# Kernel tuning notes

Hardware: AMD Instinct MI355X
Metric: run time of the kernel (lower is better)

Reference implementation:

```python
import jax, jax.numpy as jnp
import numpy as np

# --- SLAYER hyperparameters (from netParams) ---
THETA = 10.0        # spike threshold
TAU_SR = 10.0       # SRM alpha-kernel time constant (ms)
TAU_RHO = 1.0       # surrogate-gradient width
SCALE_RHO = 1.0     # surrogate-gradient scale
TS = 1.0            # simulation step (ms)
T_SAMPLE = 300      # number of time steps
K_LEN = 64          # truncated SRM kernel length

N_BATCH, N_IN, N_HID, N_OUT = 128, 784, 410, 10


def srm_kernel():
    # SRM-alpha kernel eps(t) = (t/tau) * exp(1 - t/tau), sampled at Ts, eps(0)=0
    t = jnp.arange(K_LEN, dtype=jnp.float32) * TS
    return (t / TAU_SR) * jnp.exp(1.0 - t / TAU_SR)


def psp(x):
    # Causal FIR filtering along time: out[t] = sum_k eps[k] * x[t-k]
    # x: [N, C, T]
    n, c, t = x.shape
    kern = srm_kernel()
    lhs = x.reshape(n * c, 1, t)
    rhs = kern[::-1].reshape(1, 1, K_LEN)  # flip: conv_general_dilated is cross-correlation
    out = jax.lax.conv_general_dilated(
        lhs, rhs, window_strides=(1,), padding=[(K_LEN - 1, 0)],
        dimension_numbers=("NCH", "OIH", "NCH"))
    return out.reshape(n, c, t)


@jax.custom_vjp
def spike_fn(u):
    # Heaviside threshold with surrogate gradient rho(u) = (scale/tau) * exp(-|u-theta|/tau)
    return (u >= THETA).astype(u.dtype)

def _spike_fwd(u):
    return spike_fn(u), u

def _spike_bwd(u, g):
    return (g * (SCALE_RHO / TAU_RHO) * jnp.exp(-jnp.abs(u - THETA) / TAU_RHO),)

spike_fn.defvjp(_spike_fwd, _spike_bwd)


def setup_inputs() -> dict:
    key = jax.random.key(0)
    k1, k2, k3, k4 = jax.random.split(key, 4)
    img = jax.random.uniform(k1, (N_BATCH, N_IN), dtype=jnp.float32)
    rand_u = jax.random.uniform(k2, (N_BATCH, N_IN, T_SAMPLE), dtype=jnp.float32)
    W1 = jax.random.normal(k3, (N_HID, N_IN), dtype=jnp.float32)
    W2 = jax.random.normal(k4, (N_OUT, N_HID), dtype=jnp.float32)
    return {"img": img, "rand_u": rand_u, "W1": W1, "W2": W2}


def reference(img, rand_u, W1, W2):
    # Poisson spike encoding: spike whenever uniform noise < pixel intensity
    s0 = (rand_u < img[:, :, None]).astype(jnp.float32)        # [N, 784, T]
    # fc1 (dense over spatial features, shared over time) -> psp -> spike
    a1 = jnp.einsum("nit,oi->not", s0, W1)                     # [N, 410, T]
    s1 = spike_fn(psp(a1))
    # fc2 -> psp -> spike
    a2 = jnp.einsum("nht,oh->not", s1, W2)                     # [N, 10, T]
    s2 = spike_fn(psp(a2))
    return s2
```

## Files before the change

kernel.cpp:

```cpp
#include <hip/hip_runtime.h>
#include <cstdint>
#include <cstddef>

#define N_B 128
#define N_I 784
#define N_H 410
#define N_O 10
#define TT  300
#define KL  64
#define NW  26
#define NKS 13
#define NTILES 26
#define NDIG 4
#define NKS2 7
#define S1_TILE 4800
#define S1_NSTRIDE 134400
#define SEGL 19

typedef int v4i __attribute__((ext_vector_type(4)));

__device__ __forceinline__ uint32_t expand4(uint32_t v) {
  return (v * 0x00204081u) & 0x01010101u;
}

__global__ void k_pack(const float* __restrict__ rand_u, const float* __restrict__ img,
                       uint32_t* __restrict__ s0w) {
  int t = blockIdx.x * 64 + threadIdx.x;
  int w = blockIdx.y;
  int n = blockIdx.z;
  if (t >= TT) return;
  const float* rb = rand_u + (size_t)n * N_I * TT + t;
  const float* ib = img + (size_t)n * N_I;
  int ib32 = w * 32;
  float r[32];
  #pragma unroll
  for (int b = 0; b < 32; ++b) {
    int i = ib32 + b;
    r[b] = (i < N_I) ? rb[(size_t)i * TT] : 2.0f;
  }
  uint32_t bits = 0;
  #pragma unroll
  for (int b = 0; b < 32; ++b) {
    int i = ib32 + b;
    float p = (i < N_I) ? ib[i] : 0.0f;
    bits |= (r[b] < p ? 1u : 0u) << b;
  }
  s0w[((size_t)n * TT + t) * NW + w] = bits;
}

__global__ void k_bprepall(const float* __restrict__ W1, const float* __restrict__ W2,
                           v4i* __restrict__ Bf, v4i* __restrict__ Bf2) {
  int bid  = blockIdx.x;
  int lane = threadIdx.x;
  if (bid < NDIG * NTILES * NKS) {
    int ks   = bid % NKS;
    int rest = bid / NKS;
    int nt   = rest % NTILES;
    int d    = rest / NTILES;
    int o     = nt * 16 + (lane & 15);
    int kbase = ks * 64 + (lane >> 4) * 16;
    uint32_t wds[4] = {0, 0, 0, 0};
    for (int j = 0; j < 16; ++j) {
      int k = kbase + j;
      int dig = 0;
      if (o < N_H && k < N_I) {
        double w = (double)W1[(size_t)o * N_I + k];
        int r = (int)llround(w * 268435456.0);
        for (int dd = 0; dd <= d; ++dd) {
          dig = (int)(int8_t)(uint8_t)(r & 255);
          r = (r - dig) >> 8;
        }
      }
      wds[j >> 2] |= ((uint32_t)(uint8_t)(int8_t)dig) << (8 * (j & 3));
    }
    v4i v; v[0] = (int)wds[0]; v[1] = (int)wds[1]; v[2] = (int)wds[2]; v[3] = (int)wds[3];
    Bf[(size_t)bid * 64 + lane] = v;
  } else {
    int b2 = bid - NDIG * NTILES * NKS;
    int ks = b2 % NKS2, d = b2 / NKS2;
    int o     = lane & 15;
    int kbase = ks * 64 + (lane >> 4) * 16;
    uint32_t wds[4] = {0, 0, 0, 0};
    for (int j = 0; j < 16; ++j) {
      int k = kbase + j;
      int dig = 0;
      if (o < N_O && k < N_H) {
        double w = (double)W2[(size_t)o * N_H + k];
        int r = (int)llround(w * 268435456.0);
        for (int dd = 0; dd <= d; ++dd) {
          dig = (int)(int8_t)(uint8_t)(r & 255);
          r = (r - dig) >> 8;
        }
      }
      wds[j >> 2] |= ((uint32_t)(uint8_t)(int8_t)dig) << (8 * (j & 3));
    }
    v4i v; v[0] = (int)wds[0]; v[1] = (int)wds[1]; v[2] = (int)wds[2]; v[3] = (int)wds[3];
    Bf2[(size_t)b2 * 64 + lane] = v;
  }
}

__global__ __launch_bounds__(256) void k_fused2(const uint32_t* __restrict__ s0w,
                                                const v4i* __restrict__ Bf,
                                                uint8_t* __restrict__ s1) {
  __shared__ double tile[TT][17];
  int tid = threadIdx.x;
  int wave = tid >> 6, lane = tid & 63;
  int nt = blockIdx.x, n = blockIdx.y;
  int lrow = lane & 15, quad = lane >> 4;
  int wsel = quad >> 1, hsel = (quad & 1) * 16;
  const v4i* bb = Bf + (size_t)nt * NKS * 64 + lane;
  const size_t dstr = (size_t)NTILES * NKS * 64;
  const uint32_t* srow = s0w + (size_t)n * TT * NW;

  v4i acc[5][NDIG];
  #pragma unroll
  for (int mti = 0; mti < 5; ++mti)
    #pragma unroll
    for (int d = 0; d < NDIG; ++d) { acc[mti][d][0]=0; acc[mti][d][1]=0; acc[mti][d][2]=0; acc[mti][d][3]=0; }
  int rowc[5];
  #pragma unroll
  for (int mti = 0; mti < 5; ++mti) {
    int rr = wave * 80 + mti * 16 + lrow;
    rowc[mti] = (rr > TT - 1) ? TT - 1 : rr;
  }
  v4i bcur[NDIG]; uint32_t acur[5];
  #pragma unroll
  for (int d = 0; d < NDIG; ++d) bcur[d] = bb[(size_t)d * dstr];
  #pragma unroll
  for (int mti = 0; mti < 5; ++mti) acur[mti] = srow[(size_t)rowc[mti] * NW + wsel];
  for (int ks = 0; ks < NKS; ++ks) {
    int ks2 = (ks + 1 < NKS) ? ks + 1 : ks;
    v4i bnxt[NDIG]; uint32_t anxt[5];
    #pragma unroll
    for (int d = 0; d < NDIG; ++d) bnxt[d] = bb[(size_t)d * dstr + ks2 * 64];
    #pragma unroll
    for (int mti = 0; mti < 5; ++mti) anxt[mti] = srow[(size_t)rowc[mti] * NW + ks2 * 2 + wsel];
    #pragma unroll
    for (int mti = 0; mti < 5; ++mti) {
      uint32_t h = (acur[mti] >> hsel) & 0xFFFFu;
      v4i af;
      af[0] = (int)expand4(h & 0xF);
      af[1] = (int)expand4((h >> 4) & 0xF);
      af[2] = (int)expand4((h >> 8) & 0xF);
      af[3] = (int)expand4((h >> 12) & 0xF);
      #pragma unroll
      for (int d = 0; d < NDIG; ++d)
        acc[mti][d] = __builtin_amdgcn_mfma_i32_16x16x64_i8(af, bcur[d], acc[mti][d], 0, 0, 0);
    }
    #pragma unroll
    for (int d = 0; d < NDIG; ++d) bcur[d] = bnxt[d];
    #pragma unroll
    for (int mti = 0; mti < 5; ++mti) acur[mti] = anxt[mti];
  }
  #pragma unroll
  for (int mti = 0; mti < 5; ++mti)
    #pragma unroll
    for (int r = 0; r < 4; ++r) {
      int m = wave * 80 + mti * 16 + quad * 4 + r;
      if (m < TT) {
        double v = (double)acc[mti][0][r]
                 + 256.0      * (double)acc[mti][1][r]
                 + 65536.0    * (double)acc[mti][2][r]
                 + 16777216.0 * (double)acc[mti][3][r];
        tile[m][lrow] = v;
      }
    }
  __syncthreads();

  {
    int col = tid & 15;
    int seg = tid >> 4;
    int T0 = seg * SEGL;
    int Wc = T0 - 63; if (Wc < 0) Wc = 0;
    const double q   = exp(-0.1);
    const double q64 = exp(-6.4);
    const double cS  = (exp(1.0) / 10.0) * (1.0 / 268435456.0);
    double s1a = 0.0, s2a = 0.0, s1b = 0.0, s2b = 0.0;
    uint8_t* sb = s1 + (size_t)n * S1_NSTRIDE + (size_t)nt * S1_TILE + col;
    for (int j = 0; j < 63; ++j) {
      int t = T0 - 63 + j;
      int tc = (t < 0) ? 0 : t;
      double xa = (t >= 0) ? tile[tc][col] : 0.0;
      s2a = q * (s2a + s1a);
      s1a = q * s1a + xa;
    }
    for (int j = 0; j < SEGL; ++j) {
      int t = T0 + j;
      int tc = (t > TT - 1) ? TT - 1 : t;
      int tb = t - 64;
      int tbc = (tb < 0) ? 0 : tb;
      double xa = tile[tc][col];
      double xb = (tb >= Wc) ? tile[tbc][col] : 0.0;
      s2b = q * (s2b + s1b);
      s1b = q * s1b + xb;
      s2a = q * (s2a + s1a);
      s1a = q * s1a + xa;
      double y = cS * (s2a - q64 * (s2b + 64.0 * s1b));
      if (t < TT) sb[(size_t)t * 16] = (y >= 10.0) ? 1 : 0;
    }
  }
}

__global__ __launch_bounds__(256) void k_l2f(const uint8_t* __restrict__ s1,
                                             const v4i* __restrict__ Bf2,
                                             float* __restrict__ out) {
  __shared__ double tile2[TT][17];
  int tid = threadIdx.x;
  int wave = tid >> 6, lane = tid & 63;
  int n = blockIdx.x;
  int lrow = lane & 15, quad = lane >> 4;
  const uint8_t* s1n = s1 + (size_t)n * S1_NSTRIDE;
  for (int mt = wave; mt < 19; mt += 4) {
    int m0 = mt * 16;
    int trow = m0 + lrow; if (trow > TT - 1) trow = TT - 1;
    v4i acc[NDIG];
    #pragma unroll
    for (int d = 0; d < NDIG; ++d) { acc[d][0]=0; acc[d][1]=0; acc[d][2]=0; acc[d][3]=0; }
    for (int ks = 0; ks < NKS2; ++ks) {
      v4i af = *(const v4i*)(s1n + (size_t)(ks * 4 + quad) * S1_TILE + (size_t)trow * 16);
      #pragma unroll
      for (int d = 0; d < NDIG; ++d) {
        v4i bf = Bf2[(size_t)(d * NKS2 + ks) * 64 + lane];
        acc[d] = __builtin_amdgcn_mfma_i32_16x16x64_i8(af, bf, acc[d], 0, 0, 0);
      }
    }
    #pragma unroll
    for (int r = 0; r < 4; ++r) {
      int m = m0 + quad * 4 + r;
      if (m < TT && lrow < N_O) {
        double v = (double)acc[0][r]
                 + 256.0      * (double)acc[1][r]
                 + 65536.0    * (double)acc[2][r]
                 + 16777216.0 * (double)acc[3][r];
        tile2[m][lrow] = v;
      }
    }
  }
  __syncthreads();

  {
    int col = tid & 15;
    int seg = tid >> 4;
    int T0 = seg * SEGL;
    int Wc = T0 - 63; if (Wc < 0) Wc = 0;
    const double q   = exp(-0.1);
    const double q64 = exp(-6.4);
    const double cS  = (exp(1.0) / 10.0) * (1.0 / 268435456.0);
    double s1a = 0.0, s2a = 0.0, s1b = 0.0, s2b = 0.0;
    float* ob = out + (size_t)n * N_O * TT + (size_t)col * TT;
    for (int j = 0; j < 63; ++j) {
      int t = T0 - 63 + j;
      int tc = (t < 0) ? 0 : t;
      double xa = (t >= 0) ? tile2[tc][col] : 0.0;
      s2a = q * (s2a + s1a);
      s1a = q * s1a + xa;
    }
    for (int j = 0; j < SEGL; ++j) {
      int t = T0 + j;
      int tc = (t > TT - 1) ? TT - 1 : t;
      int tb = t - 64;
      int tbc = (tb < 0) ? 0 : tb;
      double xa = tile2[tc][col];
      double xb = (tb >= Wc) ? tile2[tbc][col] : 0.0;
      s2b = q * (s2b + s1b);
      s1b = q * s1b + xb;
      s2a = q * (s2a + s1a);
      s1a = q * s1a + xa;
      double y = cS * (s2a - q64 * (s2b + 64.0 * s1b));
      if (t < TT && col < N_O) ob[t] = (y >= 10.0) ? 1.0f : 0.0f;
    }
  }
}

extern "C" void kernel_launch(void* const* d_in, const int* in_sizes, int n_in,
                              void* d_out, int out_size, void* d_ws, size_t ws_size,
                              hipStream_t stream) {
  const float* img   = (const float*)d_in[0];
  const float* randu = (const float*)d_in[1];
  const float* W1    = (const float*)d_in[2];
  const float* W2    = (const float*)d_in[3];
  float* out = (float*)d_out;

  char* ws = (char*)d_ws;
  size_t off = 0;
  auto alloc = [&](size_t bytes) -> void* {
    void* p = ws + off;
    off = (off + bytes + 511) & ~(size_t)511;
    return p;
  };
  uint32_t* s0w = (uint32_t*)alloc((size_t)N_B * TT * NW * sizeof(uint32_t));
  v4i*      Bf  = (v4i*)     alloc((size_t)NDIG * NTILES * NKS * 64 * 16);
  v4i*      Bf2 = (v4i*)     alloc((size_t)NDIG * NKS2 * 64 * 16);
  uint8_t*  s1  = (uint8_t*) alloc((size_t)N_B * S1_NSTRIDE);
  if (off > ws_size) return;

  k_pack    <<<dim3(5, NW, N_B), 64, 0, stream>>>(randu, img, s0w);
  k_bprepall<<<dim3(NDIG * NTILES * NKS + NDIG * NKS2), 64, 0, stream>>>(W1, W2, Bf, Bf2);
  k_fused2  <<<dim3(NTILES, N_B), 256, 0, stream>>>(s0w, Bf, s1);
  k_l2f     <<<dim3(N_B), 256, 0, stream>>>(s1, Bf2, out);
}
```

Before: 310.8 us.

## Store input spikes as bytes, split layer-1 MFMA pass, double layer-2 grid

The input spike tensor is now packed as one byte per input (832 per row) instead of bit-packed words. The layer-1 MFMA loop can then load int8 A fragments directly, without bit-expansion ALU work. The layer-1 pass is split into a 3-tile and a 2-tile sub-pass to reduce live accumulator registers. Layer 2 launches two blocks per batch sample, each handling half of the time segments for its PSP scan. The cost is an eightfold larger intermediate buffer, more global write and read traffic, and duplicated layer-2 MFMA work across the two halves.

```diff
diff --git a/kernel.cpp b/kernel.cpp
--- a/kernel.cpp
+++ b/kernel.cpp
@@ -8,7 +8,7 @@
 #define N_O 10
 #define TT  300
 #define KL  64
-#define NW  26
+#define NK  832
 #define NKS 13
 #define NTILES 26
 #define NDIG 4
@@ -16,36 +16,38 @@
 #define S1_TILE 4800
 #define S1_NSTRIDE 134400
 #define SEGL 19
+#define SEGL2 10
 
 typedef int v4i __attribute__((ext_vector_type(4)));
 
-__device__ __forceinline__ uint32_t expand4(uint32_t v) {
-  return (v * 0x00204081u) & 0x01010101u;
-}
-
 __global__ void k_pack(const float* __restrict__ rand_u, const float* __restrict__ img,
-                       uint32_t* __restrict__ s0w) {
+                       uint8_t* __restrict__ s0b) {
   int t = blockIdx.x * 64 + threadIdx.x;
-  int w = blockIdx.y;
+  int w2 = blockIdx.y;
   int n = blockIdx.z;
   if (t >= TT) return;
   const float* rb = rand_u + (size_t)n * N_I * TT + t;
   const float* ib = img + (size_t)n * N_I;
-  int ib32 = w * 32;
-  float r[32];
-  #pragma unroll
-  for (int b = 0; b < 32; ++b) {
-    int i = ib32 + b;
-    r[b] = (i < N_I) ? rb[(size_t)i * TT] : 2.0f;
-  }
-  uint32_t bits = 0;
-  #pragma unroll
-  for (int b = 0; b < 32; ++b) {
-    int i = ib32 + b;
-    float p = (i < N_I) ? ib[i] : 0.0f;
-    bits |= (r[b] < p ? 1u : 0u) << b;
-  }
-  s0w[((size_t)n * TT + t) * NW + w] = bits;
+  uint8_t* dst = s0b + ((size_t)n * TT + t) * NK + w2 * 64;
+  int kb = w2 * 64;
+  #pragma unroll
+  for (int g = 0; g < 4; ++g) {
+    uint32_t wd[4];
+    #pragma unroll
+    for (int q = 0; q < 4; ++q) {
+      uint32_t v = 0;
+      #pragma unroll
+      for (int b = 0; b < 4; ++b) {
+        int i = kb + g * 16 + q * 4 + b;
+        float r = (i < N_I) ? rb[(size_t)i * TT] : 2.0f;
+        float p = (i < N_I) ? ib[i] : 0.0f;
+        v |= (r < p ? 1u : 0u) << (8 * b);
+      }
+      wd[q] = v;
+    }
+    v4i o; o[0] = (int)wd[0]; o[1] = (int)wd[1]; o[2] = (int)wd[2]; o[3] = (int)wd[3];
+    *(v4i*)(dst + g * 16) = o;
+  }
 }
 
 __global__ void k_bprepall(const float* __restrict__ W1, const float* __restrict__ W2,
@@ -99,72 +101,74 @@
   }
 }
 
-__global__ __launch_bounds__(256) void k_fused2(const uint32_t* __restrict__ s0w,
+template<int NMT>
+__device__ __forceinline__ void l1_pass(const uint8_t* __restrict__ an,
+                                        const v4i* __restrict__ bb, size_t dstr,
+                                        int wave, int lane, int mt0,
+                                        double (*tile)[17]) {
+  int lrow = lane & 15, quad = lane >> 4;
+  v4i acc[NMT][NDIG];
+  #pragma unroll
+  for (int i = 0; i < NMT; ++i)
+    #pragma unroll
+    for (int d = 0; d < NDIG; ++d) { acc[i][d][0]=0; acc[i][d][1]=0; acc[i][d][2]=0; acc[i][d][3]=0; }
+  const uint8_t* ap[NMT];
+  #pragma unroll
+  for (int i = 0; i < NMT; ++i) {
+    int rr = wave * 80 + (mt0 + i) * 16 + lrow;
+    if (rr > TT - 1) rr = TT - 1;
+    ap[i] = an + (size_t)rr * NK + quad * 16;
+  }
+  v4i bcur[NDIG], acur[NMT];
+  #pragma unroll
+  for (int d = 0; d < NDIG; ++d) bcur[d] = bb[d * dstr];
+  #pragma unroll
+  for (int i = 0; i < NMT; ++i) acur[i] = *(const v4i*)ap[i];
+  for (int ks = 0; ks < NKS; ++ks) {
+    int ks2 = (ks + 1 < NKS) ? ks + 1 : ks;
+    v4i bnxt[NDIG], anxt[NMT];
+    #pragma unroll
+    for (int d = 0; d < NDIG; ++d) bnxt[d] = bb[d * dstr + ks2 * 64];
+    #pragma unroll
+    for (int i = 0; i < NMT; ++i) anxt[i] = *(const v4i*)(ap[i] + ks2 * 64);
+    #pragma unroll
+    for (int i = 0; i < NMT; ++i)
+      #pragma unroll
+      for (int d = 0; d < NDIG; ++d)
+        acc[i][d] = __builtin_amdgcn_mfma_i32_16x16x64_i8(acur[i], bcur[d], acc[i][d], 0, 0, 0);
+    #pragma unroll
+    for (int d = 0; d < NDIG; ++d) bcur[d] = bnxt[d];
+    #pragma unroll
+    for (int i = 0; i < NMT; ++i) acur[i] = anxt[i];
+  }
+  #pragma unroll
+  for (int i = 0; i < NMT; ++i)
+    #pragma unroll
+    for (int r = 0; r < 4; ++r) {
+      int m = wave * 80 + (mt0 + i) * 16 + quad * 4 + r;
+      if (m < TT) {
+        double v = (double)acc[i][0][r]
+                 + 256.0      * (double)acc[i][1][r]
+                 + 65536.0    * (double)acc[i][2][r]
+                 + 16777216.0 * (double)acc[i][3][r];
+        tile[m][lrow] = v;
+      }
+    }
+}
+
+__global__ __launch_bounds__(256) void k_fused2(const uint8_t* __restrict__ s0b,
                                                 const v4i* __restrict__ Bf,
                                                 uint8_t* __restrict__ s1) {
   __shared__ double tile[TT][17];
   int tid = threadIdx.x;
   int wave = tid >> 6, lane = tid & 63;
   int nt = blockIdx.x, n = blockIdx.y;
-  int lrow = lane & 15, quad = lane >> 4;
-  int wsel = quad >> 1, hsel = (quad & 1) * 16;
   const v4i* bb = Bf + (size_t)nt * NKS * 64 + lane;
   const size_t dstr = (size_t)NTILES * NKS * 64;
-  const uint32_t* srow = s0w + (size_t)n * TT * NW;
-
-  v4i acc[5][NDIG];
-  #pragma unroll
-  for (int mti = 0; mti < 5; ++mti)
-    #pragma unroll
-    for (int d = 0; d < NDIG; ++d) { acc[mti][d][0]=0; acc[mti][d][1]=0; acc[mti][d][2]=0; acc[mti][d][3]=0; }
-  int rowc[5];
-  #pragma unroll
-  for (int mti = 0; mti < 5; ++mti) {
-    int rr = wave * 80 + mti * 16 + lrow;
-    rowc[mti] = (rr > TT - 1) ? TT - 1 : rr;
-  }
-  v4i bcur[NDIG]; uint32_t acur[5];
-  #pragma unroll
-  for (int d = 0; d < NDIG; ++d) bcur[d] = bb[(size_t)d * dstr];
-  #pragma unroll
-  for (int mti = 0; mti < 5; ++mti) acur[mti] = srow[(size_t)rowc[mti] * NW + wsel];
-  for (int ks = 0; ks < NKS; ++ks) {
-    int ks2 = (ks + 1 < NKS) ? ks + 1 : ks;
-    v4i bnxt[NDIG]; uint32_t anxt[5];
-    #pragma unroll
-    for (int d = 0; d < NDIG; ++d) bnxt[d] = bb[(size_t)d * dstr + ks2 * 64];
-    #pragma unroll
-    for (int mti = 0; mti < 5; ++mti) anxt[mti] = srow[(size_t)rowc[mti] * NW + ks2 * 2 + wsel];
-    #pragma unroll
-    for (int mti = 0; mti < 5; ++mti) {
-      uint32_t h = (acur[mti] >> hsel) & 0xFFFFu;
-      v4i af;
-      af[0] = (int)expand4(h & 0xF);
-      af[1] = (int)expand4((h >> 4) & 0xF);
-      af[2] = (int)expand4((h >> 8) & 0xF);
-      af[3] = (int)expand4((h >> 12) & 0xF);
-      #pragma unroll
-      for (int d = 0; d < NDIG; ++d)
-        acc[mti][d] = __builtin_amdgcn_mfma_i32_16x16x64_i8(af, bcur[d], acc[mti][d], 0, 0, 0);
-    }
-    #pragma unroll
-    for (int d = 0; d < NDIG; ++d) bcur[d] = bnxt[d];
-    #pragma unroll
-    for (int mti = 0; mti < 5; ++mti) acur[mti] = anxt[mti];
-  }
-  #pragma unroll
-  for (int mti = 0; mti < 5; ++mti)
-    #pragma unroll
-    for (int r = 0; r < 4; ++r) {
-      int m = wave * 80 + mti * 16 + quad * 4 + r;
-      if (m < TT) {
-        double v = (double)acc[mti][0][r]
-                 + 256.0      * (double)acc[mti][1][r]
-                 + 65536.0    * (double)acc[mti][2][r]
-                 + 16777216.0 * (double)acc[mti][3][r];
-        tile[m][lrow] = v;
-      }
-    }
+  const uint8_t* an = s0b + (size_t)n * TT * NK;
+
+  l1_pass<3>(an, bb, dstr, wave, lane, 0, tile);
+  l1_pass<2>(an, bb, dstr, wave, lane, 3, tile);
   __syncthreads();
 
   {
@@ -207,7 +211,7 @@
   __shared__ double tile2[TT][17];
   int tid = threadIdx.x;
   int wave = tid >> 6, lane = tid & 63;
-  int n = blockIdx.x;
+  int half = blockIdx.x, n = blockIdx.y;
   int lrow = lane & 15, quad = lane >> 4;
   const uint8_t* s1n = s1 + (size_t)n * S1_NSTRIDE;
   for (int mt = wave; mt < 19; mt += 4) {
@@ -240,8 +244,8 @@
 
   {
     int col = tid & 15;
-    int seg = tid >> 4;
-    int T0 = seg * SEGL;
+    int seg = half * 16 + (tid >> 4);
+    int T0 = seg * SEGL2;
     int Wc = T0 - 63; if (Wc < 0) Wc = 0;
     const double q   = exp(-0.1);
     const double q64 = exp(-6.4);
@@ -251,15 +255,18 @@
     for (int j = 0; j < 63; ++j) {
       int t = T0 - 63 + j;
       int tc = (t < 0) ? 0 : t;
-      double xa = (t >= 0) ? tile2[tc][col] : 0.0;
+      tc = (tc > TT - 1) ? TT - 1 : tc;
+      double xa = (t >= 0 && t < TT + 63) ? tile2[tc][col] : 0.0;
+      if (t >= TT) xa = 0.0;
       s2a = q * (s2a + s1a);
       s1a = q * s1a + xa;
     }
-    for (int j = 0; j < SEGL; ++j) {
+    for (int j = 0; j < SEGL2; ++j) {
       int t = T0 + j;
       int tc = (t > TT - 1) ? TT - 1 : t;
       int tb = t - 64;
       int tbc = (tb < 0) ? 0 : tb;
+      tbc = (tbc > TT - 1) ? TT - 1 : tbc;
       double xa = tile2[tc][col];
       double xb = (tb >= Wc) ? tile2[tbc][col] : 0.0;
       s2b = q * (s2b + s1b);
@@ -288,14 +295,14 @@
     off = (off + bytes + 511) & ~(size_t)511;
     return p;
   };
-  uint32_t* s0w = (uint32_t*)alloc((size_t)N_B * TT * NW * sizeof(uint32_t));
+  uint8_t*  s0b = (uint8_t*) alloc((size_t)N_B * TT * NK);
   v4i*      Bf  = (v4i*)     alloc((size_t)NDIG * NTILES * NKS * 64 * 16);
   v4i*      Bf2 = (v4i*)     alloc((size_t)NDIG * NKS2 * 64 * 16);
   uint8_t*  s1  = (uint8_t*) alloc((size_t)N_B * S1_NSTRIDE);
   if (off > ws_size) return;
 
-  k_pack    <<<dim3(5, NW, N_B), 64, 0, stream>>>(randu, img, s0w);
+  k_pack    <<<dim3(5, NKS, N_B), 64, 0, stream>>>(randu, img, s0b);
   k_bprepall<<<dim3(NDIG * NTILES * NKS + NDIG * NKS2), 64, 0, stream>>>(W1, W2, Bf, Bf2);
-  k_fused2  <<<dim3(NTILES, N_B), 256, 0, stream>>>(s0w, Bf, s1);
-  k_l2f     <<<dim3(N_B), 256, 0, stream>>>(s1, Bf2, out);
-}
+  k_fused2  <<<dim3(NTILES, N_B), 256, 0, stream>>>(s0b, Bf, s1);
+  k_l2f     <<<dim3(2, N_B), 256, 0, stream>>>(s1, Bf2, out);
+}
```

After: 423.7 us. +36.3%, slower.
